# Performance work log

Hardware: AMD Instinct MI355X
Metric: run time of the kernel (lower is better)

The kernel has to match this reference:

```python
import jax, jax.numpy as jnp
import numpy as np

B, S, D = 2, 4096, 2048
EXPAND, K = 2, 4
DI = EXPAND * D
EPS = 1e-5


def setup_inputs() -> dict:
    key = jax.random.key(0)
    ks = jax.random.split(key, 7)
    scale = lambda d: 1.0 / np.sqrt(d)
    return {
        "x": jax.random.normal(ks[0], (B, S, D), dtype=jnp.float32),
        "w_norm": jnp.ones((D,), dtype=jnp.float32),
        "W_up": jax.random.normal(ks[1], (D, DI), dtype=jnp.float32) * scale(D),
        "W_gate": jax.random.normal(ks[2], (D, DI), dtype=jnp.float32) * scale(D),
        "W_down": jax.random.normal(ks[3], (DI, D), dtype=jnp.float32) * scale(DI),
        "conv_w": jax.random.normal(ks[4], (DI, 1, K), dtype=jnp.float32) * scale(K),
        "conv_b": jnp.zeros((DI,), dtype=jnp.float32),
    }


def _rmsnorm(x, w, eps=EPS):
    ms = jnp.mean(jnp.square(x.astype(jnp.float32)), axis=-1, keepdims=True)
    return x * jax.lax.rsqrt(ms + eps).astype(x.dtype) * w


def _causal_dwconv(h, conv_w, conv_b):
    # h: [B, S, DI] -> depthwise causal conv along S
    hc = jnp.transpose(h, (0, 2, 1))  # [B, DI, S]
    y = jax.lax.conv_general_dilated(
        hc, conv_w, window_strides=(1,), padding=[(K - 1, 0)],
        feature_group_count=DI, dimension_numbers=("NCH", "OIH", "NCH"))
    y = y + conv_b[None, :, None]
    return jnp.transpose(y, (0, 2, 1))  # [B, S, DI]


def reference(x, w_norm, W_up, W_gate, W_down, conv_w, conv_b):
    normed = _rmsnorm(x, w_norm)                       # [B,S,D]
    val = _causal_dwconv(normed @ W_up, conv_w, conv_b)  # [B,S,DI]
    gated = jax.nn.silu(normed @ W_gate) * val          # [B,S,DI]
    return x + gated @ W_down                           # [B,S,D]
```

## Files before the change

### kernel.cpp

```cpp
#include <hip/hip_runtime.h>
#include <stdint.h>

#define B_   2
#define S_   4096
#define D_   2048
#define DI_  4096
#define M_   (B_ * S_)
#define EPS_ 1e-5f
#define SCH_ 8

typedef __bf16 bf16x8 __attribute__((ext_vector_type(8)));
typedef float  f32x4  __attribute__((ext_vector_type(4)));
typedef uint16_t u16x8 __attribute__((ext_vector_type(8)));

__device__ __forceinline__ uint16_t f32_to_bf16(float f) {
    uint32_t u = __builtin_bit_cast(uint32_t, f);
    uint32_t r = (u + 0x7fffu + ((u >> 16) & 1u)) >> 16;
    return (uint16_t)r;
}
__device__ __forceinline__ float bf16_to_f32(uint16_t h) {
    return __builtin_bit_cast(float, (uint32_t)h << 16);
}

typedef const __attribute__((address_space(1))) uint32_t* gptr_t;
typedef __attribute__((address_space(3))) uint32_t* lptr_t;

__device__ __forceinline__ void gll16(const void* g, void* l) {
    __builtin_amdgcn_global_load_lds((gptr_t)g, (lptr_t)l, 16, 0, 0);
}

__global__ __launch_bounds__(256)
void transpose_bf16_kernel(const float* __restrict__ W, uint16_t* __restrict__ WT,
                           int K, int N) {
    __shared__ float tile[32][33];
    const int nb = N / 32;
    const int tn = blockIdx.x % nb;
    const int tk = blockIdx.x / nb;
    const int tx = threadIdx.x & 31;
    const int ty = threadIdx.x >> 5;
    const int gk = tk * 32, gn = tn * 32;
#pragma unroll
    for (int i = 0; i < 4; i++) {
        int k = ty + i * 8;
        tile[k][tx] = W[(size_t)(gk + k) * N + gn + tx];
    }
    __syncthreads();
#pragma unroll
    for (int i = 0; i < 4; i++) {
        int n = ty + i * 8;
        WT[(size_t)(gn + n) * K + gk + tx] = f32_to_bf16(tile[tx][n]);
    }
}

__global__ __launch_bounds__(256)
void rmsnorm_kernel(const float* __restrict__ x, const float* __restrict__ w,
                    uint16_t* __restrict__ out) {
    const int row  = blockIdx.x;
    const int tid  = threadIdx.x;
    const int lane = tid & 63, wid = tid >> 6;
    const float* xr = x + (size_t)row * D_;

    f32x4 a = *(const f32x4*)&xr[tid * 8];
    f32x4 b = *(const f32x4*)&xr[tid * 8 + 4];
    float ss = a[0]*a[0] + a[1]*a[1] + a[2]*a[2] + a[3]*a[3]
             + b[0]*b[0] + b[1]*b[1] + b[2]*b[2] + b[3]*b[3];
#pragma unroll
    for (int off = 32; off > 0; off >>= 1) ss += __shfl_xor(ss, off);

    __shared__ float red[4];
    if (lane == 0) red[wid] = ss;
    __syncthreads();
    const float tot = red[0] + red[1] + red[2] + red[3];
    const float scale = rsqrtf(tot * (1.0f / D_) + EPS_);

    f32x4 wa = *(const f32x4*)&w[tid * 8];
    f32x4 wb = *(const f32x4*)&w[tid * 8 + 4];
    u16x8 o;
#pragma unroll
    for (int j = 0; j < 4; j++) o[j]     = f32_to_bf16(a[j] * scale * wa[j]);
#pragma unroll
    for (int j = 0; j < 4; j++) o[j + 4] = f32_to_bf16(b[j] * scale * wb[j]);
    *(u16x8*)&out[(size_t)row * D_ + tid * 8] = o;
}

template <int EPI>
__global__ __launch_bounds__(512, 2)
void gemm8p_kernel(const uint16_t* __restrict__ A, const uint16_t* __restrict__ BT,
                   int M, int N, int K,
                   float* __restrict__ Cf, uint16_t* __restrict__ Cb,
                   uint16_t* __restrict__ Cb2, const float* __restrict__ resid) {
    __shared__ uint16_t As[2][16384];
    __shared__ uint16_t Bs[2][16384];

    const int nbn = N >> 8;
    const int bid = blockIdx.x;
    const int xcd = bid & 7;
    const int j   = bid >> 3;
    const int wc_ = nbn >> 3;
    const int wlog = 31 - __clz(wc_);
    const int g   = j >> 5;
    const int rr  = j & 31;
    const int bm  = g * (32 >> wlog) + (rr >> wlog);
    const int bn  = (xcd << wlog) + (rr & (wc_ - 1));

    const int brow = bm << 8, bcol = bn << 8;
    const int tid  = threadIdx.x;
    const int wid  = tid >> 6, lane = tid & 63;
    const int wr   = wid >> 2, wcv = wid & 3;
    const int fr   = lane & 15;
    const int kx0 = (((lane >> 4) << 3)) ^ ((lane & 7) << 3);
    const int kx1 = kx0 ^ 32;
    int rhoN[4];
#pragma unroll
    for (int n = 0; n < 4; n++) rhoN[n] = ((n >> 1) << 7) + (wcv << 5) + ((n & 1) << 4) + fr;

    const uint16_t* ApS[4];
    const uint16_t* BpS[4];
#pragma unroll
    for (int i = 0; i < 4; i++) {
        const int z  = (i << 13) + (wid << 10) + (lane << 4);
        const int zz = z ^ (((z >> 7) & 7) << 4);
        const int row = zz >> 7;
        const int kk  = (zz >> 1) & 63;
        ApS[i] = A + (size_t)(brow + row) * K + kk;
        const int h = row >> 7, q = (row >> 5) & 3, jj = row & 31;
        BpS[i] = BT + (size_t)(bcol + q * 64 + h * 32 + jj) * K + kk;
    }

    f32x4 acc[8][4];
#pragma unroll
    for (int i = 0; i < 8; i++)
#pragma unroll
        for (int jn = 0; jn < 4; jn++) acc[i][jn] = (f32x4){0.f, 0.f, 0.f, 0.f};

    const int nt = K >> 6;

#pragma unroll
    for (int i = 0; i < 4; i++) gll16(ApS[i], &As[0][i * 4096 + wid * 512]);
#pragma unroll
    for (int i = 0; i < 4; i++) gll16(BpS[i], &Bs[0][i * 4096 + wid * 512]);
    asm volatile("s_waitcnt vmcnt(0)" ::: "memory");
    __builtin_amdgcn_s_barrier();

    bf16x8 aF[8], bF[8];

    for (int t = 0; t < nt; ++t) {
        const int cur = t & 1, nxt = cur ^ 1;
        const int kn  = (t + 1) << 6;
        const bool pf = (t + 1) < nt;

#pragma unroll
        for (int mh = 0; mh < 4; ++mh) {
            const int r = (wr << 7) + (mh << 4) + fr;
            aF[mh * 2 + 0] = *(const bf16x8*)&As[cur][r * 64 + kx0];
            aF[mh * 2 + 1] = *(const bf16x8*)&As[cur][r * 64 + kx1];
        }
#pragma unroll
        for (int n = 0; n < 2; ++n) {
            bF[n * 2 + 0] = *(const bf16x8*)&Bs[cur][rhoN[n] * 64 + kx0];
            bF[n * 2 + 1] = *(const bf16x8*)&Bs[cur][rhoN[n] * 64 + kx1];
        }
        if (pf) {
            gll16(ApS[0] + kn, &As[nxt][0 * 4096 + wid * 512]);
            gll16(ApS[2] + kn, &As[nxt][2 * 4096 + wid * 512]);
        }
        __builtin_amdgcn_s_barrier();
        __builtin_amdgcn_s_setprio(1);
#pragma unroll
        for (int mh = 0; mh < 4; ++mh)
#pragma unroll
            for (int n = 0; n < 2; ++n)
#pragma unroll
                for (int ks = 0; ks < 2; ++ks)
                    acc[mh][n] = __builtin_amdgcn_mfma_f32_16x16x32_bf16(
                        aF[mh * 2 + ks], bF[n * 2 + ks], acc[mh][n], 0, 0, 0);
        __builtin_amdgcn_s_setprio(0);
        asm volatile("s_waitcnt vmcnt(4)" ::: "memory");
        __builtin_amdgcn_s_barrier();

#pragma unroll
        for (int n = 2; n < 4; ++n) {
            bF[n * 2 + 0] = *(const bf16x8*)&Bs[cur][rhoN[n] * 64 + kx0];
            bF[n * 2 + 1] = *(const bf16x8*)&Bs[cur][rhoN[n] * 64 + kx1];
        }
        if (pf) {
            gll16(BpS[0] + kn, &Bs[nxt][0 * 4096 + wid * 512]);
            gll16(BpS[1] + kn, &Bs[nxt][1 * 4096 + wid * 512]);
        }
        __builtin_amdgcn_s_barrier();
        __builtin_amdgcn_s_setprio(1);
#pragma unroll
        for (int mh = 0; mh < 4; ++mh)
#pragma unroll
            for (int n = 2; n < 4; ++n)
#pragma unroll
                for (int ks = 0; ks < 2; ++ks)
                    acc[mh][n] = __builtin_amdgcn_mfma_f32_16x16x32_bf16(
                        aF[mh * 2 + ks], bF[n * 2 + ks], acc[mh][n], 0, 0, 0);
        __builtin_amdgcn_s_setprio(0);
        asm volatile("s_waitcnt vmcnt(4)" ::: "memory");
        __builtin_amdgcn_s_barrier();

#pragma unroll
        for (int mh = 0; mh < 4; ++mh) {
            const int r = (wr << 7) + 64 + (mh << 4) + fr;
            aF[mh * 2 + 0] = *(const bf16x8*)&As[cur][r * 64 + kx0];
            aF[mh * 2 + 1] = *(const bf16x8*)&As[cur][r * 64 + kx1];
        }
        if (pf) {
            gll16(BpS[2] + kn, &Bs[nxt][2 * 4096 + wid * 512]);
            gll16(BpS[3] + kn, &Bs[nxt][3 * 4096 + wid * 512]);
        }
        __builtin_amdgcn_s_barrier();
        __builtin_amdgcn_s_setprio(1);
#pragma unroll
        for (int mh = 0; mh < 4; ++mh)
#pragma unroll
            for (int n = 2; n < 4; ++n)
#pragma unroll
                for (int ks = 0; ks < 2; ++ks)
                    acc[4 + mh][n] = __builtin_amdgcn_mfma_f32_16x16x32_bf16(
                        aF[mh * 2 + ks], bF[n * 2 + ks], acc[4 + mh][n], 0, 0, 0);
        __builtin_amdgcn_s_setprio(0);
        __builtin_amdgcn_s_barrier();

        if (pf) {
            gll16(ApS[1] + kn, &As[nxt][1 * 4096 + wid * 512]);
            gll16(ApS[3] + kn, &As[nxt][3 * 4096 + wid * 512]);
        }
        __builtin_amdgcn_s_barrier();
        __builtin_amdgcn_s_setprio(1);
#pragma unroll
        for (int mh = 0; mh < 4; ++mh)
#pragma unroll
            for (int n = 0; n < 2; ++n)
#pragma unroll
                for (int ks = 0; ks < 2; ++ks)
                    acc[4 + mh][n] = __builtin_amdgcn_mfma_f32_16x16x32_bf16(
                        aF[mh * 2 + ks], bF[n * 2 + ks], acc[4 + mh][n], 0, 0, 0);
        __builtin_amdgcn_s_setprio(0);
        asm volatile("s_waitcnt vmcnt(4)" ::: "memory");
        __builtin_amdgcn_s_barrier();
    }

    const int r0 = (lane >> 4) << 2;
    const bool upHalf = (bcol < DI_);
#pragma unroll
    for (int m = 0; m < 8; ++m) {
        const int row = brow + (wr << 7) + ((m >> 2) << 6) + ((m & 3) << 4) + r0;
#pragma unroll
        for (int n = 0; n < 4; ++n) {
            const int col = bcol + (wcv << 6) + (n << 4) + fr;
#pragma unroll
            for (int r = 0; r < 4; ++r) {
                const float v = acc[m][n][r];
                if (EPI == 0) {
                    const size_t idx = (size_t)(row + r) * N + col;
                    Cf[idx] = v + resid[idx];
                } else {
                    if (upHalf) {
                        Cb[(size_t)(row + r) * DI_ + col] = f32_to_bf16(v);
                    } else {
                        const float s = v / (1.0f + __expf(-v));
                        Cb2[(size_t)(row + r) * DI_ + (col - DI_)] = f32_to_bf16(s);
                    }
                }
            }
        }
    }
}

__global__ __launch_bounds__(256)
void conv_mul_kernel(const uint16_t* __restrict__ up, uint16_t* __restrict__ sg,
                     const float* __restrict__ cw, const float* __restrict__ cb) {
    const size_t gid = (size_t)blockIdx.x * 256 + threadIdx.x;
    const int c8 = (int)(gid % (DI_ / 8));
    const int sc = (int)((gid / (DI_ / 8)) % (S_ / SCH_));
    const int b  = (int)(gid / ((size_t)(DI_ / 8) * (S_ / SCH_)));
    const int c0 = c8 * 8;
    const int s0 = sc * SCH_;

    f32x4 wv[8];
#pragma unroll
    for (int j = 0; j < 8; j++) wv[j] = *(const f32x4*)&cw[(c0 + j) * 4];
    const f32x4 b0 = *(const f32x4*)&cb[c0];
    const f32x4 b1 = *(const f32x4*)&cb[c0 + 4];

    const uint16_t* upb = up + (size_t)b * S_ * DI_ + c0;
    uint16_t*       sgb = sg + (size_t)b * S_ * DI_ + c0;

    u16x8 win[3];
#pragma unroll
    for (int i = 0; i < 3; i++) {
        const int ss = s0 - 3 + i;
        if (ss >= 0) {
            win[i] = *(const u16x8*)&upb[(size_t)ss * DI_];
        } else {
#pragma unroll
            for (int j = 0; j < 8; j++) win[i][j] = 0;
        }
    }

#pragma unroll
    for (int st = 0; st < SCH_; ++st) {
        const size_t roff = (size_t)(s0 + st) * DI_;
        const u16x8 curv = *(const u16x8*)&upb[roff];
        const u16x8 gv   = *(const u16x8*)&sgb[roff];
        u16x8 o;
#pragma unroll
        for (int j = 0; j < 8; j++) {
            const float bias = (j < 4) ? b0[j] : b1[j - 4];
            const float a = bias
                + bf16_to_f32(win[0][j]) * wv[j][0]
                + bf16_to_f32(win[1][j]) * wv[j][1]
                + bf16_to_f32(win[2][j]) * wv[j][2]
                + bf16_to_f32(curv[j])   * wv[j][3];
            o[j] = f32_to_bf16(bf16_to_f32(gv[j]) * a);
        }
        *(u16x8*)&sgb[roff] = o;
        win[0] = win[1]; win[1] = win[2]; win[2] = curv;
    }
}

extern "C" void kernel_launch(void* const* d_in, const int* in_sizes, int n_in,
                              void* d_out, int out_size, void* d_ws, size_t ws_size,
                              hipStream_t stream) {
    const float* x      = (const float*)d_in[0];
    const float* w_norm = (const float*)d_in[1];
    const float* W_up   = (const float*)d_in[2];
    const float* W_gate = (const float*)d_in[3];
    const float* W_down = (const float*)d_in[4];
    const float* conv_w = (const float*)d_in[5];
    const float* conv_b = (const float*)d_in[6];
    float* out = (float*)d_out;

    char* ws = (char*)d_ws;
    uint16_t* normed = (uint16_t*)ws;  ws += (size_t)M_  * D_  * 2;
    uint16_t* WupT   = (uint16_t*)ws;  ws += (size_t)DI_ * D_  * 2;
    uint16_t* WgateT = (uint16_t*)ws;  ws += (size_t)DI_ * D_  * 2;
    uint16_t* WdownT = (uint16_t*)ws;  ws += (size_t)D_  * DI_ * 2;
    uint16_t* up     = (uint16_t*)ws;  ws += (size_t)M_  * DI_ * 2;
    uint16_t* sg     = (uint16_t*)ws;  ws += (size_t)M_  * DI_ * 2;

    transpose_bf16_kernel<<<(D_ / 32) * (DI_ / 32), 256, 0, stream>>>(W_up,   WupT,   D_,  DI_);
    transpose_bf16_kernel<<<(D_ / 32) * (DI_ / 32), 256, 0, stream>>>(W_gate, WgateT, D_,  DI_);
    transpose_bf16_kernel<<<(DI_ / 32) * (D_ / 32), 256, 0, stream>>>(W_down, WdownT, DI_, D_);

    rmsnorm_kernel<<<M_, 256, 0, stream>>>(x, w_norm, normed);

    gemm8p_kernel<3><<<(M_ / 256) * ((2 * DI_) / 256), 512, 0, stream>>>(
        normed, WupT, M_, 2 * DI_, D_, nullptr, up, sg, nullptr);

    conv_mul_kernel<<<(int)(((size_t)B_ * (S_ / SCH_) * (DI_ / 8)) / 256), 256, 0, stream>>>(
        up, sg, conv_w, conv_b);

    gemm8p_kernel<0><<<(M_ / 256) * (D_ / 256), 512, 0, stream>>>(
        sg, WdownT, M_, D_, DI_, out, nullptr, nullptr, x);
}
```

Before: 511.0 us.

## Register double-buffer fragments and deepen B prefetch in GEMM main loop

```diff
diff --git a/kernel.cpp b/kernel.cpp
--- a/kernel.cpp
+++ b/kernel.cpp
@@ -113,19 +113,17 @@
     int rhoN[4];
 #pragma unroll
     for (int n = 0; n < 4; n++) rhoN[n] = ((n >> 1) << 7) + (wcv << 5) + ((n & 1) << 4) + fr;
-
-    const uint16_t* ApS[4];
-    const uint16_t* BpS[4];
-#pragma unroll
-    for (int i = 0; i < 4; i++) {
-        const int z  = (i << 13) + (wid << 10) + (lane << 4);
-        const int zz = z ^ (((z >> 7) & 7) << 4);
-        const int row = zz >> 7;
-        const int kk  = (zz >> 1) & 63;
-        ApS[i] = A + (size_t)(brow + row) * K + kk;
-        const int h = row >> 7, q = (row >> 5) & 3, jj = row & 31;
-        BpS[i] = BT + (size_t)(bcol + q * 64 + h * 32 + jj) * K + kk;
-    }
+    const int rA0 = (wr << 7) + fr;
+
+    const int z0  = (wid << 10) + (lane << 4);
+    const int zz0 = z0 ^ (((z0 >> 7) & 7) << 4);
+    const int row0 = zz0 >> 7;
+    const int kk0  = (zz0 >> 1) & 63;
+    const uint16_t* Ap0 = A + (size_t)(brow + row0) * K + kk0;
+    const uint16_t* Bp0 = BT + (size_t)(bcol + (row0 >> 5) * 64 + (row0 & 31)) * K + kk0;
+    const size_t sA  = (size_t)64 * K;
+    const size_t rB1 = (size_t)128 * K, rB2 = (size_t)32 * K, rB3 = (size_t)160 * K;
+    const int ldsL = wid * 512;
 
     f32x4 acc[8][4];
 #pragma unroll
@@ -135,113 +133,89 @@
 
     const int nt = K >> 6;
 
-#pragma unroll
-    for (int i = 0; i < 4; i++) gll16(ApS[i], &As[0][i * 4096 + wid * 512]);
-#pragma unroll
-    for (int i = 0; i < 4; i++) gll16(BpS[i], &Bs[0][i * 4096 + wid * 512]);
-    asm volatile("s_waitcnt vmcnt(0)" ::: "memory");
+    bf16x8 aA[8], aB[8], bh0[4], bh1[4];
+
+#define LD_A(DST, BUF, H1)  _Pragma("unroll") \
+    for (int mh = 0; mh < 4; ++mh) { \
+        const int rr_ = (rA0 + (H1) + (mh << 4)) * 64; \
+        DST[mh * 2 + 0] = *(const bf16x8*)&BUF[rr_ + kx0]; \
+        DST[mh * 2 + 1] = *(const bf16x8*)&BUF[rr_ + kx1]; }
+#define LD_B(DST, BUF, NB)  _Pragma("unroll") \
+    for (int n2 = 0; n2 < 2; ++n2) { \
+        const int rr_ = rhoN[(NB) + n2] * 64; \
+        DST[n2 * 2 + 0] = *(const bf16x8*)&BUF[rr_ + kx0]; \
+        DST[n2 * 2 + 1] = *(const bf16x8*)&BUF[rr_ + kx1]; }
+#define MM(AR, BR, M0, N0)  _Pragma("unroll") \
+    for (int mh = 0; mh < 4; ++mh) _Pragma("unroll") \
+    for (int n2 = 0; n2 < 2; ++n2) _Pragma("unroll") \
+    for (int ks = 0; ks < 2; ++ks) \
+        acc[(M0) + mh][(N0) + n2] = __builtin_amdgcn_mfma_f32_16x16x32_bf16( \
+            AR[mh * 2 + ks], BR[n2 * 2 + ks], acc[(M0) + mh][(N0) + n2], 0, 0, 0);
+
+    gll16(Ap0,            &As[0][0 * 4096 + ldsL]);
+    gll16(Ap0 + 2 * sA,   &As[0][2 * 4096 + ldsL]);
+    gll16(Bp0,            &Bs[0][0 * 4096 + ldsL]);
+    gll16(Bp0 + rB1,      &Bs[0][1 * 4096 + ldsL]);
+    gll16(Bp0 + rB2,      &Bs[0][2 * 4096 + ldsL]);
+    gll16(Bp0 + rB3,      &Bs[0][3 * 4096 + ldsL]);
+    gll16(Ap0 + sA,       &As[0][1 * 4096 + ldsL]);
+    gll16(Ap0 + 3 * sA,   &As[0][3 * 4096 + ldsL]);
+    gll16(Bp0 + 64,       &Bs[1][0 * 4096 + ldsL]);
+    gll16(Bp0 + rB1 + 64, &Bs[1][1 * 4096 + ldsL]);
+    asm volatile("s_waitcnt vmcnt(4)" ::: "memory");
     __builtin_amdgcn_s_barrier();
-
-    bf16x8 aF[8], bF[8];
+    LD_A(aA, As[0], 0)
+    LD_B(bh0, Bs[0], 0)
+    LD_B(bh1, Bs[0], 2)
 
     for (int t = 0; t < nt; ++t) {
         const int cur = t & 1, nxt = cur ^ 1;
-        const int kn  = (t + 1) << 6;
-        const bool pf = (t + 1) < nt;
-
-#pragma unroll
-        for (int mh = 0; mh < 4; ++mh) {
-            const int r = (wr << 7) + (mh << 4) + fr;
-            aF[mh * 2 + 0] = *(const bf16x8*)&As[cur][r * 64 + kx0];
-            aF[mh * 2 + 1] = *(const bf16x8*)&As[cur][r * 64 + kx1];
-        }
-#pragma unroll
-        for (int n = 0; n < 2; ++n) {
-            bF[n * 2 + 0] = *(const bf16x8*)&Bs[cur][rhoN[n] * 64 + kx0];
-            bF[n * 2 + 1] = *(const bf16x8*)&Bs[cur][rhoN[n] * 64 + kx1];
-        }
-        if (pf) {
-            gll16(ApS[0] + kn, &As[nxt][0 * 4096 + wid * 512]);
-            gll16(ApS[2] + kn, &As[nxt][2 * 4096 + wid * 512]);
-        }
+        const int kn1 = (t + 1) << 6;
+        const int kn2 = (t + 2) << 6;
+
+        gll16(Ap0 + kn1,          &As[nxt][0 * 4096 + ldsL]);
+        gll16(Ap0 + 2 * sA + kn1, &As[nxt][2 * 4096 + ldsL]);
         __builtin_amdgcn_s_barrier();
         __builtin_amdgcn_s_setprio(1);
-#pragma unroll
-        for (int mh = 0; mh < 4; ++mh)
-#pragma unroll
-            for (int n = 0; n < 2; ++n)
-#pragma unroll
-                for (int ks = 0; ks < 2; ++ks)
-                    acc[mh][n] = __builtin_amdgcn_mfma_f32_16x16x32_bf16(
-                        aF[mh * 2 + ks], bF[n * 2 + ks], acc[mh][n], 0, 0, 0);
+        MM(aA, bh0, 0, 0)
         __builtin_amdgcn_s_setprio(0);
         asm volatile("s_waitcnt vmcnt(4)" ::: "memory");
         __builtin_amdgcn_s_barrier();
 
-#pragma unroll
-        for (int n = 2; n < 4; ++n) {
-            bF[n * 2 + 0] = *(const bf16x8*)&Bs[cur][rhoN[n] * 64 + kx0];
-            bF[n * 2 + 1] = *(const bf16x8*)&Bs[cur][rhoN[n] * 64 + kx1];
-        }
-        if (pf) {
-            gll16(BpS[0] + kn, &Bs[nxt][0 * 4096 + wid * 512]);
-            gll16(BpS[1] + kn, &Bs[nxt][1 * 4096 + wid * 512]);
-        }
+        LD_A(aB, As[cur], 64)
+        gll16(Bp0 + rB2 + kn1, &Bs[nxt][2 * 4096 + ldsL]);
+        gll16(Bp0 + rB3 + kn1, &Bs[nxt][3 * 4096 + ldsL]);
         __builtin_amdgcn_s_barrier();
         __builtin_amdgcn_s_setprio(1);
-#pragma unroll
-        for (int mh = 0; mh < 4; ++mh)
-#pragma unroll
-            for (int n = 2; n < 4; ++n)
-#pragma unroll
-                for (int ks = 0; ks < 2; ++ks)
-                    acc[mh][n] = __builtin_amdgcn_mfma_f32_16x16x32_bf16(
-                        aF[mh * 2 + ks], bF[n * 2 + ks], acc[mh][n], 0, 0, 0);
+        MM(aA, bh1, 0, 2)
         __builtin_amdgcn_s_setprio(0);
+        asm volatile("s_waitcnt vmcnt(2)" ::: "memory");
+        __builtin_amdgcn_s_barrier();
+
+        LD_A(aA, As[nxt], 0)
+        gll16(Ap0 + sA + kn1,     &As[nxt][1 * 4096 + ldsL]);
+        gll16(Ap0 + 3 * sA + kn1, &As[nxt][3 * 4096 + ldsL]);
+        __builtin_amdgcn_s_barrier();
+        __builtin_amdgcn_s_setprio(1);
+        MM(aB, bh1, 4, 2)
+        __builtin_amdgcn_s_setprio(0);
+        asm volatile("s_waitcnt vmcnt(2)" ::: "memory");
+        __builtin_amdgcn_s_barrier();
+
+        LD_B(bh1, Bs[nxt], 2)
+        gll16(Bp0 + kn2,       &Bs[cur][0 * 4096 + ldsL]);
+        gll16(Bp0 + rB1 + kn2, &Bs[cur][1 * 4096 + ldsL]);
+        __builtin_amdgcn_s_barrier();
+        __builtin_amdgcn_s_setprio(1);
+        MM(aB, bh0, 4, 0)
+        __builtin_amdgcn_s_setprio(0);
+        LD_B(bh0, Bs[nxt], 0)
         asm volatile("s_waitcnt vmcnt(4)" ::: "memory");
         __builtin_amdgcn_s_barrier();
-
-#pragma unroll
-        for (int mh = 0; mh < 4; ++mh) {
-            const int r = (wr << 7) + 64 + (mh << 4) + fr;
-            aF[mh * 2 + 0] = *(const bf16x8*)&As[cur][r * 64 + kx0];
-            aF[mh * 2 + 1] = *(const bf16x8*)&As[cur][r * 64 + kx1];
-        }
-        if (pf) {
-            gll16(BpS[2] + kn, &Bs[nxt][2 * 4096 + wid * 512]);
-            gll16(BpS[3] + kn, &Bs[nxt][3 * 4096 + wid * 512]);
-        }
-        __builtin_amdgcn_s_barrier();
-        __builtin_amdgcn_s_setprio(1);
-#pragma unroll
-        for (int mh = 0; mh < 4; ++mh)
-#pragma unroll
-            for (int n = 2; n < 4; ++n)
-#pragma unroll
-                for (int ks = 0; ks < 2; ++ks)
-                    acc[4 + mh][n] = __builtin_amdgcn_mfma_f32_16x16x32_bf16(
-                        aF[mh * 2 + ks], bF[n * 2 + ks], acc[4 + mh][n], 0, 0, 0);
-        __builtin_amdgcn_s_setprio(0);
-        __builtin_amdgcn_s_barrier();
-
-        if (pf) {
-            gll16(ApS[1] + kn, &As[nxt][1 * 4096 + wid * 512]);
-            gll16(ApS[3] + kn, &As[nxt][3 * 4096 + wid * 512]);
-        }
-        __builtin_amdgcn_s_barrier();
-        __builtin_amdgcn_s_setprio(1);
-#pragma unroll
-        for (int mh = 0; mh < 4; ++mh)
-#pragma unroll
-            for (int n = 0; n < 2; ++n)
-#pragma unroll
-                for (int ks = 0; ks < 2; ++ks)
-                    acc[4 + mh][n] = __builtin_amdgcn_mfma_f32_16x16x32_bf16(
-                        aF[mh * 2 + ks], bF[n * 2 + ks], acc[4 + mh][n], 0, 0, 0);
-        __builtin_amdgcn_s_setprio(0);
-        asm volatile("s_waitcnt vmcnt(4)" ::: "memory");
-        __builtin_amdgcn_s_barrier();
-    }
+    }
+#undef LD_A
+#undef LD_B
+#undef MM
 
     const int r0 = (lane >> 4) << 2;
     const bool upHalf = (bcol < DI_);
```

Measured after the change: 589.6 us. 1.15x slower.

## Deepen GEMM prefetch to two K-tiles ahead with 2x-unrolled main loop

Applied to the files above, without the earlier changes.

```diff
diff --git a/kernel.cpp b/kernel.cpp
--- a/kernel.cpp
+++ b/kernel.cpp
@@ -126,6 +126,7 @@
         const int h = row >> 7, q = (row >> 5) & 3, jj = row & 31;
         BpS[i] = BT + (size_t)(bcol + q * 64 + h * 32 + jj) * K + kk;
     }
+    const int ldsL = wid * 512;
 
     f32x4 acc[8][4];
 #pragma unroll
@@ -133,115 +134,110 @@
 #pragma unroll
         for (int jn = 0; jn < 4; jn++) acc[i][jn] = (f32x4){0.f, 0.f, 0.f, 0.f};
 
-    const int nt = K >> 6;
-
-#pragma unroll
-    for (int i = 0; i < 4; i++) gll16(ApS[i], &As[0][i * 4096 + wid * 512]);
-#pragma unroll
-    for (int i = 0; i < 4; i++) gll16(BpS[i], &Bs[0][i * 4096 + wid * 512]);
-    asm volatile("s_waitcnt vmcnt(0)" ::: "memory");
+    const int nt  = K >> 6;
+    const int nit = nt >> 1;
+
+    gll16(ApS[0],      &As[0][0 * 4096 + ldsL]);
+    gll16(ApS[2],      &As[0][2 * 4096 + ldsL]);
+    gll16(BpS[0],      &Bs[0][0 * 4096 + ldsL]);
+    gll16(BpS[1],      &Bs[0][1 * 4096 + ldsL]);
+    gll16(BpS[2],      &Bs[0][2 * 4096 + ldsL]);
+    gll16(BpS[3],      &Bs[0][3 * 4096 + ldsL]);
+    gll16(ApS[1],      &As[0][1 * 4096 + ldsL]);
+    gll16(ApS[3],      &As[0][3 * 4096 + ldsL]);
+    gll16(ApS[0] + 64, &As[1][0 * 4096 + ldsL]);
+    gll16(ApS[2] + 64, &As[1][2 * 4096 + ldsL]);
+    gll16(BpS[2] + 64, &Bs[1][2 * 4096 + ldsL]);
+    gll16(BpS[3] + 64, &Bs[1][3 * 4096 + ldsL]);
+    gll16(ApS[1] + 64, &As[1][1 * 4096 + ldsL]);
+    gll16(ApS[3] + 64, &As[1][3 * 4096 + ldsL]);
+    asm volatile("s_waitcnt vmcnt(6)" ::: "memory");
     __builtin_amdgcn_s_barrier();
 
     bf16x8 aF[8], bF[8];
 
-    for (int t = 0; t < nt; ++t) {
-        const int cur = t & 1, nxt = cur ^ 1;
-        const int kn  = (t + 1) << 6;
-        const bool pf = (t + 1) < nt;
-
-#pragma unroll
-        for (int mh = 0; mh < 4; ++mh) {
-            const int r = (wr << 7) + (mh << 4) + fr;
-            aF[mh * 2 + 0] = *(const bf16x8*)&As[cur][r * 64 + kx0];
-            aF[mh * 2 + 1] = *(const bf16x8*)&As[cur][r * 64 + kx1];
-        }
-#pragma unroll
-        for (int n = 0; n < 2; ++n) {
-            bF[n * 2 + 0] = *(const bf16x8*)&Bs[cur][rhoN[n] * 64 + kx0];
-            bF[n * 2 + 1] = *(const bf16x8*)&Bs[cur][rhoN[n] * 64 + kx1];
-        }
-        if (pf) {
-            gll16(ApS[0] + kn, &As[nxt][0 * 4096 + wid * 512]);
-            gll16(ApS[2] + kn, &As[nxt][2 * 4096 + wid * 512]);
-        }
-        __builtin_amdgcn_s_barrier();
-        __builtin_amdgcn_s_setprio(1);
-#pragma unroll
-        for (int mh = 0; mh < 4; ++mh)
-#pragma unroll
-            for (int n = 0; n < 2; ++n)
-#pragma unroll
-                for (int ks = 0; ks < 2; ++ks)
-                    acc[mh][n] = __builtin_amdgcn_mfma_f32_16x16x32_bf16(
-                        aF[mh * 2 + ks], bF[n * 2 + ks], acc[mh][n], 0, 0, 0);
-        __builtin_amdgcn_s_setprio(0);
-        asm volatile("s_waitcnt vmcnt(4)" ::: "memory");
-        __builtin_amdgcn_s_barrier();
-
-#pragma unroll
-        for (int n = 2; n < 4; ++n) {
-            bF[n * 2 + 0] = *(const bf16x8*)&Bs[cur][rhoN[n] * 64 + kx0];
-            bF[n * 2 + 1] = *(const bf16x8*)&Bs[cur][rhoN[n] * 64 + kx1];
-        }
-        if (pf) {
-            gll16(BpS[0] + kn, &Bs[nxt][0 * 4096 + wid * 512]);
-            gll16(BpS[1] + kn, &Bs[nxt][1 * 4096 + wid * 512]);
-        }
-        __builtin_amdgcn_s_barrier();
-        __builtin_amdgcn_s_setprio(1);
-#pragma unroll
-        for (int mh = 0; mh < 4; ++mh)
-#pragma unroll
-            for (int n = 2; n < 4; ++n)
-#pragma unroll
-                for (int ks = 0; ks < 2; ++ks)
-                    acc[mh][n] = __builtin_amdgcn_mfma_f32_16x16x32_bf16(
-                        aF[mh * 2 + ks], bF[n * 2 + ks], acc[mh][n], 0, 0, 0);
-        __builtin_amdgcn_s_setprio(0);
-        asm volatile("s_waitcnt vmcnt(4)" ::: "memory");
-        __builtin_amdgcn_s_barrier();
-
-#pragma unroll
-        for (int mh = 0; mh < 4; ++mh) {
-            const int r = (wr << 7) + 64 + (mh << 4) + fr;
-            aF[mh * 2 + 0] = *(const bf16x8*)&As[cur][r * 64 + kx0];
-            aF[mh * 2 + 1] = *(const bf16x8*)&As[cur][r * 64 + kx1];
-        }
-        if (pf) {
-            gll16(BpS[2] + kn, &Bs[nxt][2 * 4096 + wid * 512]);
-            gll16(BpS[3] + kn, &Bs[nxt][3 * 4096 + wid * 512]);
-        }
-        __builtin_amdgcn_s_barrier();
-        __builtin_amdgcn_s_setprio(1);
-#pragma unroll
-        for (int mh = 0; mh < 4; ++mh)
-#pragma unroll
-            for (int n = 2; n < 4; ++n)
-#pragma unroll
-                for (int ks = 0; ks < 2; ++ks)
-                    acc[4 + mh][n] = __builtin_amdgcn_mfma_f32_16x16x32_bf16(
-                        aF[mh * 2 + ks], bF[n * 2 + ks], acc[4 + mh][n], 0, 0, 0);
-        __builtin_amdgcn_s_setprio(0);
-        __builtin_amdgcn_s_barrier();
-
-        if (pf) {
-            gll16(ApS[1] + kn, &As[nxt][1 * 4096 + wid * 512]);
-            gll16(ApS[3] + kn, &As[nxt][3 * 4096 + wid * 512]);
-        }
-        __builtin_amdgcn_s_barrier();
-        __builtin_amdgcn_s_setprio(1);
-#pragma unroll
-        for (int mh = 0; mh < 4; ++mh)
-#pragma unroll
-            for (int n = 0; n < 2; ++n)
-#pragma unroll
-                for (int ks = 0; ks < 2; ++ks)
-                    acc[4 + mh][n] = __builtin_amdgcn_mfma_f32_16x16x32_bf16(
-                        aF[mh * 2 + ks], bF[n * 2 + ks], acc[4 + mh][n], 0, 0, 0);
-        __builtin_amdgcn_s_setprio(0);
-        asm volatile("s_waitcnt vmcnt(4)" ::: "memory");
-        __builtin_amdgcn_s_barrier();
-    }
+#define RD_A(BUFC, H1) _Pragma("unroll") \
+    for (int mh = 0; mh < 4; ++mh) { \
+        const int r_ = ((wr << 7) + (H1) + (mh << 4) + fr) * 64; \
+        aF[mh * 2 + 0] = *(const bf16x8*)&As[BUFC][r_ + kx0]; \
+        aF[mh * 2 + 1] = *(const bf16x8*)&As[BUFC][r_ + kx1]; }
+#define RD_B(BUFC, NB) _Pragma("unroll") \
+    for (int n2 = (NB); n2 < (NB) + 2; ++n2) { \
+        const int r_ = rhoN[n2] * 64; \
+        bF[n2 * 2 + 0] = *(const bf16x8*)&Bs[BUFC][r_ + kx0]; \
+        bF[n2 * 2 + 1] = *(const bf16x8*)&Bs[BUFC][r_ + kx1]; }
+#define MM(M0, N0) _Pragma("unroll") \
+    for (int mh = 0; mh < 4; ++mh) _Pragma("unroll") \
+    for (int n2 = 0; n2 < 2; ++n2) _Pragma("unroll") \
+    for (int ks = 0; ks < 2; ++ks) \
+        acc[(M0) + mh][(N0) + n2] = __builtin_amdgcn_mfma_f32_16x16x32_bf16( \
+            aF[mh * 2 + ks], bF[((N0) + n2) * 2 + ks], acc[(M0) + mh][(N0) + n2], 0, 0, 0);
+#define BAR __builtin_amdgcn_s_barrier()
+#define PRI(x) __builtin_amdgcn_s_setprio(x)
+
+    for (int it = 0; it < nit; ++it) {
+        const bool last = (it == nit - 1);
+
+        RD_A(0, 0) RD_B(0, 0)
+        gll16(BpS[0] + 64, &Bs[1][0 * 4096 + ldsL]);
+        gll16(BpS[1] + 64, &Bs[1][1 * 4096 + ldsL]);
+        BAR; PRI(1); MM(0, 0) PRI(0); BAR;
+        RD_B(0, 2)
+        if (!last) {
+            gll16(ApS[0] + 128, &As[0][0 * 4096 + ldsL]);
+            gll16(ApS[2] + 128, &As[0][2 * 4096 + ldsL]);
+        }
+        BAR; PRI(1); MM(0, 2) PRI(0); BAR;
+        RD_A(0, 64)
+        if (!last) {
+            gll16(BpS[2] + 128, &Bs[0][2 * 4096 + ldsL]);
+            gll16(BpS[3] + 128, &Bs[0][3 * 4096 + ldsL]);
+        }
+        BAR; PRI(1); MM(4, 2) PRI(0); BAR;
+        if (!last) {
+            gll16(ApS[1] + 128, &As[0][1 * 4096 + ldsL]);
+            gll16(ApS[3] + 128, &As[0][3 * 4096 + ldsL]);
+        }
+        BAR; PRI(1); MM(4, 0) PRI(0);
+        if (!last) { asm volatile("s_waitcnt vmcnt(6)" ::: "memory"); }
+        else       { asm volatile("s_waitcnt vmcnt(0)" ::: "memory"); }
+        BAR;
+
+        RD_A(1, 0) RD_B(1, 0)
+        if (!last) {
+            gll16(BpS[0] + 128, &Bs[0][0 * 4096 + ldsL]);
+            gll16(BpS[1] + 128, &Bs[0][1 * 4096 + ldsL]);
+        }
+        BAR; PRI(1); MM(0, 0) PRI(0); BAR;
+        RD_B(1, 2)
+        if (!last) {
+            gll16(ApS[0] + 192, &As[1][0 * 4096 + ldsL]);
+            gll16(ApS[2] + 192, &As[1][2 * 4096 + ldsL]);
+        }
+        BAR; PRI(1); MM(0, 2) PRI(0); BAR;
+        RD_A(1, 64)
+        if (!last) {
+            gll16(BpS[2] + 192, &Bs[1][2 * 4096 + ldsL]);
+            gll16(BpS[3] + 192, &Bs[1][3 * 4096 + ldsL]);
+        }
+        BAR; PRI(1); MM(4, 2) PRI(0); BAR;
+        if (!last) {
+            gll16(ApS[1] + 192, &As[1][1 * 4096 + ldsL]);
+            gll16(ApS[3] + 192, &As[1][3 * 4096 + ldsL]);
+        }
+        BAR; PRI(1); MM(4, 0) PRI(0);
+        if (!last) { asm volatile("s_waitcnt vmcnt(6)" ::: "memory"); }
+        else       { asm volatile("s_waitcnt vmcnt(0)" ::: "memory"); }
+        BAR;
+
+#pragma unroll
+        for (int i = 0; i < 4; i++) { ApS[i] += 128; BpS[i] += 128; }
+    }
+#undef RD_A
+#undef RD_B
+#undef MM
+#undef BAR
+#undef PRI
 
     const int r0 = (lane >> 4) << 2;
     const bool upHalf = (bcol < DI_);
```

After: 538.3 us. 5.3% more time.
